# Performance work log

Hardware: AMD Instinct MI355X
Metric: run time of the kernel (lower is better)

Reference implementation:

```python
import jax, jax.numpy as jnp
import numpy as np

EPS = 1e-6
NUM_HEADS = 16

def rmsnorm(x, w):
    # x: [..., d], w: [d]
    norm = jax.lax.rsqrt(jnp.mean(x * x, axis=-1, keepdims=True) + EPS)
    return w * (x * norm)

def setup_inputs() -> dict:
    key = jax.random.key(0)
    ks = jax.random.split(key, 6)
    B, N, C = 2, 2048, 1024
    H = NUM_HEADS
    hd = C // H
    x = jax.random.normal(ks[0], (B, N, C), dtype=jnp.float32)
    scale = 1.0 / np.sqrt(C)
    qkv_w = jax.random.normal(ks[1], (C, 3 * C), dtype=jnp.float32) * scale
    qkv_b = jnp.zeros((3 * C,), dtype=jnp.float32)
    q_norm_w = jnp.ones((hd,), dtype=jnp.float32)
    k_norm_w = jnp.ones((hd,), dtype=jnp.float32)
    proj_w = jax.random.normal(ks[2], (C, C), dtype=jnp.float32) * scale
    proj_b = jnp.zeros((C,), dtype=jnp.float32)
    return {"x": x, "qkv_w": qkv_w, "qkv_b": qkv_b,
            "q_norm_w": q_norm_w, "k_norm_w": k_norm_w,
            "proj_w": proj_w, "proj_b": proj_b}

def reference(x, qkv_w, qkv_b, q_norm_w, k_norm_w, proj_w, proj_b):
    B, N, C = x.shape
    H = NUM_HEADS
    hd = C // H
    qkv = x @ qkv_w + qkv_b                       # [B,N,3C]
    qkv = qkv.reshape(B, N, 3, H, hd)
    q, k, v = qkv[:, :, 0], qkv[:, :, 1], qkv[:, :, 2]  # [B,N,H,hd]
    q = jnp.transpose(q, (0, 2, 1, 3))            # [B,H,N,hd]
    k = jnp.transpose(k, (0, 2, 1, 3))
    v = jnp.transpose(v, (0, 2, 1, 3))
    q = rmsnorm(q, q_norm_w)
    k = rmsnorm(k, k_norm_w)
    scores = jnp.einsum('bhqd,bhkd->bhqk', q, k) / jnp.sqrt(jnp.float32(hd))
    attn = jax.nn.softmax(scores, axis=-1)
    out = jnp.einsum('bhqk,bhkd->bhqd', attn, v)  # [B,H,N,hd]
    out = jnp.transpose(out, (0, 2, 1, 3)).reshape(B, N, C)
    return out @ proj_w + proj_b
```

## Files before the change

### kernel.cpp

```cpp
#include <hip/hip_runtime.h>

typedef unsigned short u16;
typedef unsigned int u32;
typedef __bf16 bf16x8 __attribute__((ext_vector_type(8)));
typedef float f32x4 __attribute__((ext_vector_type(4)));
typedef unsigned short u16x8 __attribute__((ext_vector_type(8)));
typedef unsigned short u16x4 __attribute__((ext_vector_type(4)));

__device__ __forceinline__ float bf2f(u16 u) {
    union { unsigned int i; float f; } c; c.i = ((unsigned int)u) << 16; return c.f;
}
__device__ __forceinline__ u16 f2bf(float f) {
    union { float f; unsigned int i; } c; c.f = f;
    unsigned int r = c.i + 0x7FFFu + ((c.i >> 16) & 1u);
    return (u16)(r >> 16);
}
__device__ __forceinline__ u16 f2bf_rtz(float f) {
    union { float f; unsigned int i; } c; c.f = f;
    return (u16)(c.i >> 16);
}
__device__ __forceinline__ float fast_exp2(float x) {
#if __has_builtin(__builtin_amdgcn_exp2f)
    return __builtin_amdgcn_exp2f(x);
#else
    return exp2f(x);
#endif
}
__device__ __forceinline__ bf16x8 u2b(u16x8 v) {
    return __builtin_bit_cast(bf16x8, v);
}
__device__ __forceinline__ void async16(const void* g, void* l) {
    __builtin_amdgcn_global_load_lds(
        (const __attribute__((address_space(1))) u32*)g,
        (__attribute__((address_space(3))) u32*)l, 16, 0, 0);
}

__global__ __launch_bounds__(256) void prep(
    const float* __restrict__ X, u16* __restrict__ Xb,
    const float* __restrict__ qkv_w, u16* __restrict__ qwT,
    const float* __restrict__ proj_w, u16* __restrict__ pwT)
{
    __shared__ float tile[32][33];
    const int blk = blockIdx.x;
    const int t = threadIdx.x;
    if (blk < 2048) {
        const size_t i = ((size_t)blk * 256 + t) * 8;
        u16x8 h;
        #pragma unroll
        for (int e = 0; e < 8; ++e) h[e] = f2bf(X[i + e]);
        *(u16x8*)&Xb[i] = h;
        return;
    }
    const float* W; u16* Th; int K, N, bx, by;
    if (blk < 5120) {
        W = qkv_w; Th = qwT; K = 1024; N = 3072;
        bx = (blk - 2048) % 96; by = (blk - 2048) / 96;
    } else {
        W = proj_w; Th = pwT; K = 1024; N = 1024;
        bx = (blk - 5120) % 32; by = (blk - 5120) / 32;
    }
    const int bk = by * 32, bn = bx * 32;
    const int tx = t & 31, ty = t >> 5;
    #pragma unroll
    for (int r = ty; r < 32; r += 8)
        tile[r][tx] = W[(size_t)(bk + r) * N + bn + tx];
    __syncthreads();
    if (t < 128) {
        const int row = t >> 2;
        const int c8 = (t & 3) * 8;
        u16x8 h;
        #pragma unroll
        for (int e = 0; e < 8; ++e) h[e] = f2bf(tile[c8 + e][row]);
        *(u16x8*)&Th[(size_t)(bn + row) * K + bk + c8] = h;
    }
}

__global__ __launch_bounds__(256) void gemm_qkv(
    const u16* __restrict__ AH, const u16* __restrict__ BH,
    const float* __restrict__ bias,
    u16* __restrict__ Qb, u16* __restrict__ Kb, u16* __restrict__ Vt,
    const float* __restrict__ qw, const float* __restrict__ kw)
{
    const int K = 1024;
    __shared__ __align__(16) u16 AhT[2 * 128 * 32];
    __shared__ __align__(16) u16 BhT[2 * 128 * 32];
    const int t = threadIdx.x;
    const int bm = blockIdx.y * 128, bn = blockIdx.x * 128;
    const int wave = t >> 6, lane = t & 63;
    const int wm = (wave >> 1) * 64, wn = (wave & 1) * 64;
    const int l15 = lane & 15, quad = lane >> 4;
    const int srow = lane >> 2;
    const int scol = (((lane & 3) ^ ((lane >> 3) & 3))) * 8;
    const int rq = (quad ^ ((l15 >> 1) & 3)) * 8;

    f32x4 acc[4][4];
    const f32x4 zero = {0.0f, 0.0f, 0.0f, 0.0f};
    #pragma unroll
    for (int i = 0; i < 4; ++i)
        #pragma unroll
        for (int j = 0; j < 4; ++j) acc[i][j] = zero;

    for (int k0 = 0; k0 < K; k0 += 64) {
        #pragma unroll
        for (int s = 0; s < 2; ++s) {
            const int kk = k0 + s * 32;
            #pragma unroll
            for (int rr = 0; rr < 2; ++rr) {
                const int r0 = (rr * 4 + wave) * 16;
                async16(&AH[(size_t)(bm + r0 + srow) * K + kk + scol],
                        &AhT[s * 4096 + r0 * 32]);
                async16(&BH[(size_t)(bn + r0 + srow) * K + kk + scol],
                        &BhT[s * 4096 + r0 * 32]);
            }
        }
        __syncthreads();
        #pragma unroll
        for (int s = 0; s < 2; ++s) {
            const int sb = s * 4096;
            bf16x8 ah[4], bh[4];
            #pragma unroll
            for (int i = 0; i < 4; ++i)
                ah[i] = *(const bf16x8*)&AhT[sb + (wm + i * 16 + l15) * 32 + rq];
            #pragma unroll
            for (int j = 0; j < 4; ++j)
                bh[j] = *(const bf16x8*)&BhT[sb + (wn + j * 16 + l15) * 32 + rq];
            #pragma unroll
            for (int i = 0; i < 4; ++i)
                #pragma unroll
                for (int j = 0; j < 4; ++j)
                    acc[i][j] = __builtin_amdgcn_mfma_f32_16x16x32_bf16(
                        ah[i], bh[j], acc[i][j], 0, 0, 0);
        }
        __syncthreads();
    }

    const int gc0 = bn + wn;
    const int sec = gc0 >> 10;
    const int h = (gc0 & 1023) >> 6;
    const int b = bm >> 11;
    const int bhd = b * 16 + h;
    float bv[4], wj[4];
    #pragma unroll
    for (int j = 0; j < 4; ++j) {
        const int d = j * 16 + l15;
        bv[j] = bias[gc0 + d];
        wj[j] = (sec == 2) ? 0.0f : (sec ? kw[d] : qw[d] * 0.18033688011f);
    }
    if (sec < 2) {
        u16* dst = sec ? Kb : Qb;
        #pragma unroll
        for (int i = 0; i < 4; ++i) {
            float val[4][4];
            float ss[4] = {0.0f, 0.0f, 0.0f, 0.0f};
            #pragma unroll
            for (int j = 0; j < 4; ++j)
                #pragma unroll
                for (int r = 0; r < 4; ++r) {
                    val[j][r] = acc[i][j][r] + bv[j];
                    ss[r] += val[j][r] * val[j][r];
                }
            #pragma unroll
            for (int r = 0; r < 4; ++r) {
                #pragma unroll
                for (int m = 1; m < 16; m <<= 1)
                    ss[r] += __shfl_xor(ss[r], m, 64);
                const float nrm = rsqrtf(ss[r] * 0.015625f + 1e-6f);
                const int n = (bm + wm + i * 16 + quad * 4 + r) & 2047;
                const size_t rowb = ((size_t)bhd * 2048 + n) * 64;
                u16x4 pk;
                #pragma unroll
                for (int j = 0; j < 4; ++j)
                    pk[j] = f2bf(val[j][r] * nrm * wj[j]);
                *(u16x4*)&dst[rowb + l15 * 4] = pk;
            }
        }
    } else {
        const int nb = (bm + wm) & 2047;
        #pragma unroll
        for (int i = 0; i < 4; ++i) {
            const int s0 = (i & 1) * 32 + quad * 8 + (i >> 1) * 4;
            #pragma unroll
            for (int j = 0; j < 4; ++j) {
                const int d = j * 16 + l15;
                u16x4 pk;
                #pragma unroll
                for (int r = 0; r < 4; ++r)
                    pk[r] = f2bf(acc[i][j][r] + bv[j]);
                *(u16x4*)&Vt[((size_t)bhd * 64 + d) * 2048 + nb + s0] = pk;
            }
        }
    }
}

__global__ __launch_bounds__(256) void gemm_proj(
    const u16* __restrict__ AH, const u16* __restrict__ BH,
    const float* __restrict__ bias, float* __restrict__ C)
{
    const int N = 1024, K = 1024;
    __shared__ __align__(16) u16 AhT[4 * 64 * 32];
    __shared__ __align__(16) u16 BhT[4 * 128 * 32];
    const int t = threadIdx.x;
    const int bm = blockIdx.y * 64, bn = blockIdx.x * 128;
    const int wave = t >> 6, lane = t & 63;
    const int l15 = lane & 15, quad = lane >> 4;
    const int srow = lane >> 2;
    const int scol = (((lane & 3) ^ ((lane >> 3) & 3))) * 8;
    const int rq = (quad ^ ((l15 >> 1) & 3)) * 8;

    f32x4 acc[4][2];
    const f32x4 zero = {0.0f, 0.0f, 0.0f, 0.0f};
    #pragma unroll
    for (int i = 0; i < 4; ++i)
        #pragma unroll
        for (int j = 0; j < 2; ++j) acc[i][j] = zero;

    for (int k0 = 0; k0 < K; k0 += 128) {
        #pragma unroll
        for (int s = 0; s < 4; ++s) {
            const int kk = k0 + s * 32;
            {
                const int r0 = wave * 16;
                async16(&AH[(size_t)(bm + r0 + srow) * K + kk + scol],
                        &AhT[s * 2048 + r0 * 32]);
            }
            #pragma unroll
            for (int cc = 0; cc < 2; ++cc) {
                const int r0 = (wave * 2 + cc) * 16;
                async16(&BH[(size_t)(bn + r0 + srow) * K + kk + scol],
                        &BhT[s * 4096 + r0 * 32]);
            }
        }
        __syncthreads();
        #pragma unroll
        for (int s = 0; s < 4; ++s) {
            const int ab = s * 2048, bb = s * 4096;
            bf16x8 ah[4], bh[2];
            #pragma unroll
            for (int i = 0; i < 4; ++i)
                ah[i] = *(const bf16x8*)&AhT[ab + (i * 16 + l15) * 32 + rq];
            #pragma unroll
            for (int j = 0; j < 2; ++j)
                bh[j] = *(const bf16x8*)
                    &BhT[bb + (wave * 32 + j * 16 + l15) * 32 + rq];
            #pragma unroll
            for (int i = 0; i < 4; ++i)
                #pragma unroll
                for (int j = 0; j < 2; ++j)
                    acc[i][j] = __builtin_amdgcn_mfma_f32_16x16x32_bf16(
                        ah[i], bh[j], acc[i][j], 0, 0, 0);
        }
        __syncthreads();
    }

    #pragma unroll
    for (int j = 0; j < 2; ++j) {
        const int col = bn + wave * 32 + j * 16 + l15;
        const float bv = bias[col];
        #pragma unroll
        for (int i = 0; i < 4; ++i) {
            const int row = bm + i * 16 + quad * 4;
            #pragma unroll
            for (int r = 0; r < 4; ++r)
                C[(size_t)(row + r) * N + col] = acc[i][j][r] + bv;
        }
    }
}

__global__ __launch_bounds__(512) void flash_attn_mfma(
    const u16* __restrict__ Qb, const u16* __restrict__ Kb,
    const u16* __restrict__ Vt, u16* __restrict__ Attn)
{
    __shared__ __align__(16) u16 Klds[2 * 64 * 64];
    __shared__ __align__(16) u16 Vlds[2 * 64 * 64];

    const int t = threadIdx.x;
    const int bid = blockIdx.x;
    const int bh = bid & 31;
    const int qt = bid >> 5;
    const int n0 = qt * 256;
    const size_t kbase = (size_t)bh * 2048 * 64;
    const size_t vbase = (size_t)bh * 64 * 2048;
    const int wave = t >> 6, lane = t & 63;
    const int l15 = lane & 15, quad = lane >> 4;
    const int srow8 = lane >> 3;
    const int sgrp = lane & 7;

    bf16x8 qf[2][2];
    #pragma unroll
    for (int qs = 0; qs < 2; ++qs) {
        const size_t qrow =
            ((size_t)bh * 2048 + n0 + wave * 32 + qs * 16 + l15) * 64;
        qf[qs][0] = *(const bf16x8*)&Qb[qrow + quad * 8];
        qf[qs][1] = *(const bf16x8*)&Qb[qrow + 32 + quad * 8];
    }

    int kofs[4][2];
    #pragma unroll
    for (int nt = 0; nt < 4; ++nt) {
        const int row = nt * 16 + l15;
        kofs[nt][0] = row * 64 + ((quad ^ (row & 7)) * 8);
        kofs[nt][1] = row * 64 + (((quad + 4) ^ (row & 7)) * 8);
    }

    f32x4 o[2][4];
    const f32x4 zero = {0.0f, 0.0f, 0.0f, 0.0f};
    #pragma unroll
    for (int qs = 0; qs < 2; ++qs)
        #pragma unroll
        for (int dt = 0; dt < 4; ++dt) o[qs][dt] = zero;
    f32x4 osum[2] = {zero, zero};
    bf16x8 ones;
    #pragma unroll
    for (int e = 0; e < 8; ++e) ones[e] = (__bf16)1.0f;

    {
        const int r0 = wave * 8;
        const int row = r0 + srow8;
        const int gg = sgrp ^ (row & 7);
        async16(&Kb[kbase + (size_t)row * 64 + gg * 8], &Klds[r0 * 64]);
        async16(&Vt[vbase + (size_t)row * 2048 + gg * 8], &Vlds[r0 * 64]);
    }

    for (int kt = 0; kt < 32; ++kt) {
        __syncthreads();
        if (kt + 1 < 32) {
            const int nb = ((kt + 1) & 1) * 4096;
            const int r0 = wave * 8;
            const int row = r0 + srow8;
            const int gg = sgrp ^ (row & 7);
            async16(&Kb[kbase + (size_t)((kt + 1) * 64 + row) * 64 + gg * 8],
                    &Klds[nb + r0 * 64]);
            async16(&Vt[vbase + (size_t)row * 2048 + (kt + 1) * 64 + gg * 8],
                    &Vlds[nb + r0 * 64]);
        }
        const int cb = (kt & 1) * 4096;

        f32x4 s[2][4];
        #pragma unroll
        for (int nt = 0; nt < 4; ++nt) {
            bf16x8 kf0 = *(const bf16x8*)&Klds[cb + kofs[nt][0]];
            bf16x8 kf1 = *(const bf16x8*)&Klds[cb + kofs[nt][1]];
            #pragma unroll
            for (int qs = 0; qs < 2; ++qs) {
                s[qs][nt] = __builtin_amdgcn_mfma_f32_16x16x32_bf16(
                    kf0, qf[qs][0], zero, 0, 0, 0);
                s[qs][nt] = __builtin_amdgcn_mfma_f32_16x16x32_bf16(
                    kf1, qf[qs][1], s[qs][nt], 0, 0, 0);
            }
        }

        bf16x8 pf[2][2];
        #pragma unroll
        for (int qs = 0; qs < 2; ++qs) {
            #pragma unroll
            for (int m = 0; m < 2; ++m) {
                u16x8 pk;
                #pragma unroll
                for (int r = 0; r < 4; ++r) {
                    pk[r]     = f2bf_rtz(fast_exp2(s[qs][m][r]));
                    pk[4 + r] = f2bf_rtz(fast_exp2(s[qs][m + 2][r]));
                }
                pf[qs][m] = u2b(pk);
            }
        }

        #pragma unroll
        for (int dt = 0; dt < 4; ++dt) {
            bf16x8 vf0 = *(const bf16x8*)&Vlds[cb + kofs[dt][0]];
            bf16x8 vf1 = *(const bf16x8*)&Vlds[cb + kofs[dt][1]];
            #pragma unroll
            for (int qs = 0; qs < 2; ++qs) {
                o[qs][dt] = __builtin_amdgcn_mfma_f32_16x16x32_bf16(
                    pf[qs][0], vf0, o[qs][dt], 0, 0, 0);
                o[qs][dt] = __builtin_amdgcn_mfma_f32_16x16x32_bf16(
                    pf[qs][1], vf1, o[qs][dt], 0, 0, 0);
            }
        }
        #pragma unroll
        for (int qs = 0; qs < 2; ++qs) {
            osum[qs] = __builtin_amdgcn_mfma_f32_16x16x32_bf16(
                pf[qs][0], ones, osum[qs], 0, 0, 0);
            osum[qs] = __builtin_amdgcn_mfma_f32_16x16x32_bf16(
                pf[qs][1], ones, osum[qs], 0, 0, 0);
        }
    }

    const size_t obase =
        ((size_t)(bh >> 4) * 2048 + n0) * 1024 + (bh & 15) * 64;
    #pragma unroll
    for (int qs = 0; qs < 2; ++qs)
        #pragma unroll
        for (int r = 0; r < 4; ++r) {
            const float inv = 1.0f / osum[qs][r];
            const size_t rbase =
                obase + (size_t)(wave * 32 + qs * 16 + quad * 4 + r) * 1024;
            #pragma unroll
            for (int dt = 0; dt < 4; ++dt)
                Attn[rbase + dt * 16 + l15] = f2bf(o[qs][dt][r] * inv);
        }
}

extern "C" void kernel_launch(void* const* d_in, const int* in_sizes, int n_in,
                              void* d_out, int out_size, void* d_ws, size_t ws_size,
                              hipStream_t stream)
{
    const float* x      = (const float*)d_in[0];
    const float* qkv_w  = (const float*)d_in[1];
    const float* qkv_b  = (const float*)d_in[2];
    const float* q_nw   = (const float*)d_in[3];
    const float* k_nw   = (const float*)d_in[4];
    const float* proj_w = (const float*)d_in[5];
    const float* proj_b = (const float*)d_in[6];
    float* out = (float*)d_out;

    char* ws = (char*)d_ws;
    u16* AttnB = (u16*)ws;
    u16* qwT   = (u16*)(ws + 8388608);
    u16* pwT   = (u16*)(ws + 14680064);
    u16* Xb    = (u16*)(ws + 16777216);
    u16* QbB   = (u16*)(ws + 25165824);
    u16* KbB   = (u16*)(ws + 33554432);
    u16* VtB   = (u16*)(ws + 41943040);
    (void)in_sizes; (void)n_in; (void)out_size;
    if (ws_size < 50331648u) return;

    prep<<<dim3(6144), 256, 0, stream>>>(x, Xb, qkv_w, qwT, proj_w, pwT);
    gemm_qkv<<<dim3(3072 / 128, 4096 / 128), 256, 0, stream>>>(
        Xb, qwT, qkv_b, QbB, KbB, VtB, q_nw, k_nw);
    flash_attn_mfma<<<dim3(256), 512, 0, stream>>>(QbB, KbB, VtB, AttnB);
    gemm_proj<<<dim3(1024 / 128, 4096 / 64), 256, 0, stream>>>(
        AttnB, pwT, proj_b, out);
}
```

Baseline: 195.2 us.

## Enlarge QKV GEMM tiles to 256x256 with double-buffered async prefetch

Reworks the QKV projection GEMM to use 256x256 output tiles with 512 threads (8 waves, each computing 128x64). The K loop now double-buffers 32-wide slices in LDS, prefetching two steps ahead with explicit vmcnt waits, so global loads overlap with MFMA work instead of stalling at every chunk. Larger tiles raise arithmetic intensity but cut the grid to 192 blocks and double per-thread accumulators, which may reduce occupancy and leave CUs idle.

```diff
diff --git a/kernel.cpp b/kernel.cpp
--- a/kernel.cpp
+++ b/kernel.cpp
@@ -75,63 +75,77 @@
     }
 }
 
-__global__ __launch_bounds__(256) void gemm_qkv(
+__global__ __launch_bounds__(512, 2) void gemm_qkv(
     const u16* __restrict__ AH, const u16* __restrict__ BH,
     const float* __restrict__ bias,
     u16* __restrict__ Qb, u16* __restrict__ Kb, u16* __restrict__ Vt,
     const float* __restrict__ qw, const float* __restrict__ kw)
 {
     const int K = 1024;
-    __shared__ __align__(16) u16 AhT[2 * 128 * 32];
-    __shared__ __align__(16) u16 BhT[2 * 128 * 32];
+    __shared__ __align__(16) u16 AhT[2 * 256 * 32];
+    __shared__ __align__(16) u16 BhT[2 * 256 * 32];
     const int t = threadIdx.x;
-    const int bm = blockIdx.y * 128, bn = blockIdx.x * 128;
+    const int bm = blockIdx.y * 256, bn = blockIdx.x * 256;
     const int wave = t >> 6, lane = t & 63;
-    const int wm = (wave >> 1) * 64, wn = (wave & 1) * 64;
+    const int wm = (wave >> 2) * 128, wn = (wave & 3) * 64;
     const int l15 = lane & 15, quad = lane >> 4;
     const int srow = lane >> 2;
     const int scol = (((lane & 3) ^ ((lane >> 3) & 3))) * 8;
     const int rq = (quad ^ ((l15 >> 1) & 3)) * 8;
 
-    f32x4 acc[4][4];
+    f32x4 acc[8][4];
     const f32x4 zero = {0.0f, 0.0f, 0.0f, 0.0f};
     #pragma unroll
-    for (int i = 0; i < 4; ++i)
-        #pragma unroll
-        for (int j = 0; j < 4; ++j) acc[i][j] = zero;
-
-    for (int k0 = 0; k0 < K; k0 += 64) {
-        #pragma unroll
-        for (int s = 0; s < 2; ++s) {
-            const int kk = k0 + s * 32;
-            #pragma unroll
-            for (int rr = 0; rr < 2; ++rr) {
-                const int r0 = (rr * 4 + wave) * 16;
+    for (int mi = 0; mi < 8; ++mi)
+        #pragma unroll
+        for (int nj = 0; nj < 4; ++nj) acc[mi][nj] = zero;
+
+    #pragma unroll
+    for (int ps = 0; ps < 2; ++ps)
+        #pragma unroll
+        for (int g = 0; g < 2; ++g) {
+            const int r0 = (g * 8 + wave) * 16;
+            async16(&AH[(size_t)(bm + r0 + srow) * K + ps * 32 + scol],
+                    &AhT[ps * 8192 + r0 * 32]);
+            async16(&BH[(size_t)(bn + r0 + srow) * K + ps * 32 + scol],
+                    &BhT[ps * 8192 + r0 * 32]);
+        }
+
+    for (int ks = 0; ks < 32; ++ks) {
+        if (ks == 31) asm volatile("s_waitcnt vmcnt(0)" ::: "memory");
+        else          asm volatile("s_waitcnt vmcnt(4)" ::: "memory");
+        __builtin_amdgcn_sched_barrier(0);
+        __builtin_amdgcn_s_barrier();
+
+        const int cb = (ks & 1) * 8192;
+        bf16x8 ah[8], bh[4];
+        #pragma unroll
+        for (int mi = 0; mi < 8; ++mi)
+            ah[mi] = *(const bf16x8*)&AhT[cb + (wm + mi * 16 + l15) * 32 + rq];
+        #pragma unroll
+        for (int nj = 0; nj < 4; ++nj)
+            bh[nj] = *(const bf16x8*)&BhT[cb + (wn + nj * 16 + l15) * 32 + rq];
+        #pragma unroll
+        for (int mi = 0; mi < 8; ++mi)
+            #pragma unroll
+            for (int nj = 0; nj < 4; ++nj)
+                acc[mi][nj] = __builtin_amdgcn_mfma_f32_16x16x32_bf16(
+                    ah[mi], bh[nj], acc[mi][nj], 0, 0, 0);
+
+        __builtin_amdgcn_sched_barrier(0);
+        __builtin_amdgcn_s_barrier();
+        if (ks + 2 < 32) {
+            const int kk = (ks + 2) * 32;
+            #pragma unroll
+            for (int g = 0; g < 2; ++g) {
+                const int r0 = (g * 8 + wave) * 16;
                 async16(&AH[(size_t)(bm + r0 + srow) * K + kk + scol],
-                        &AhT[s * 4096 + r0 * 32]);
+                        &AhT[cb + r0 * 32]);
                 async16(&BH[(size_t)(bn + r0 + srow) * K + kk + scol],
-                        &BhT[s * 4096 + r0 * 32]);
-            }
-        }
-        __syncthreads();
-        #pragma unroll
-        for (int s = 0; s < 2; ++s) {
-            const int sb = s * 4096;
-            bf16x8 ah[4], bh[4];
-            #pragma unroll
-            for (int i = 0; i < 4; ++i)
-                ah[i] = *(const bf16x8*)&AhT[sb + (wm + i * 16 + l15) * 32 + rq];
-            #pragma unroll
-            for (int j = 0; j < 4; ++j)
-                bh[j] = *(const bf16x8*)&BhT[sb + (wn + j * 16 + l15) * 32 + rq];
-            #pragma unroll
-            for (int i = 0; i < 4; ++i)
-                #pragma unroll
-                for (int j = 0; j < 4; ++j)
-                    acc[i][j] = __builtin_amdgcn_mfma_f32_16x16x32_bf16(
-                        ah[i], bh[j], acc[i][j], 0, 0, 0);
-        }
-        __syncthreads();
+                        &BhT[cb + r0 * 32]);
+            }
+            __builtin_amdgcn_sched_barrier(0);
+        }
     }
 
     const int gc0 = bn + wn;
@@ -149,14 +163,14 @@
     if (sec < 2) {
         u16* dst = sec ? Kb : Qb;
         #pragma unroll
-        for (int i = 0; i < 4; ++i) {
+        for (int mi = 0; mi < 8; ++mi) {
             float val[4][4];
             float ss[4] = {0.0f, 0.0f, 0.0f, 0.0f};
             #pragma unroll
             for (int j = 0; j < 4; ++j)
                 #pragma unroll
                 for (int r = 0; r < 4; ++r) {
-                    val[j][r] = acc[i][j][r] + bv[j];
+                    val[j][r] = acc[mi][j][r] + bv[j];
                     ss[r] += val[j][r] * val[j][r];
                 }
             #pragma unroll
@@ -165,7 +179,7 @@
                 for (int m = 1; m < 16; m <<= 1)
                     ss[r] += __shfl_xor(ss[r], m, 64);
                 const float nrm = rsqrtf(ss[r] * 0.015625f + 1e-6f);
-                const int n = (bm + wm + i * 16 + quad * 4 + r) & 2047;
+                const int n = (bm + wm + mi * 16 + quad * 4 + r) & 2047;
                 const size_t rowb = ((size_t)bhd * 2048 + n) * 64;
                 u16x4 pk;
                 #pragma unroll
@@ -175,9 +189,10 @@
             }
         }
     } else {
-        const int nb = (bm + wm) & 2047;
-        #pragma unroll
-        for (int i = 0; i < 4; ++i) {
+        #pragma unroll
+        for (int mi = 0; mi < 8; ++mi) {
+            const int i = mi & 3;
+            const int nb = (bm + wm + (mi >> 2) * 64) & 2047;
             const int s0 = (i & 1) * 32 + quad * 8 + (i >> 1) * 4;
             #pragma unroll
             for (int j = 0; j < 4; ++j) {
@@ -185,7 +200,7 @@
                 u16x4 pk;
                 #pragma unroll
                 for (int r = 0; r < 4; ++r)
-                    pk[r] = f2bf(acc[i][j][r] + bv[j]);
+                    pk[r] = f2bf(acc[mi][j][r] + bv[j]);
                 *(u16x4*)&Vt[((size_t)bhd * 64 + d) * 2048 + nb + s0] = pk;
             }
         }
@@ -425,7 +440,7 @@
     if (ws_size < 50331648u) return;
 
     prep<<<dim3(6144), 256, 0, stream>>>(x, Xb, qkv_w, qwT, proj_w, pwT);
-    gemm_qkv<<<dim3(3072 / 128, 4096 / 128), 256, 0, stream>>>(
+    gemm_qkv<<<dim3(3072 / 256, 4096 / 256), 512, 0, stream>>>(
         Xb, qwT, qkv_b, QbB, KbB, VtB, q_nw, k_nw);
     flash_attn_mfma<<<dim3(256), 512, 0, stream>>>(QbB, KbB, VtB, AttnB);
     gemm_proj<<<dim3(1024 / 128, 4096 / 64), 256, 0, stream>>>(
```

Result: no change. 193.9 us (-0.7%).
